# Kernel tuning notes

Measured on AMD Instinct MI355X. Metric: run time of the kernel, lower is better.

The kernel has to match this reference:

```python
import jax, jax.numpy as jnp
import numpy as np

T, H, W, N = 16, 1280, 1280, 64

def setup_inputs() -> dict:
    key = jax.random.key(0)
    k1, k2, k3 = jax.random.split(key, 3)
    result_data = jax.random.normal(k1, (T, H, W), dtype=jnp.float32)
    # boxes: (x1, y1, x2, y2) with x1 <= x2, y1 <= y2 (well-formed, as the torch code assumes)
    xs = jnp.sort(jax.random.randint(k2, (N, 2), 0, W, dtype=jnp.int32), axis=1)
    ys = jnp.sort(jax.random.randint(k3, (N, 2), 0, H, dtype=jnp.int32), axis=1)
    boxes_data = jnp.stack([xs[:, 0], ys[:, 0], xs[:, 1], ys[:, 1]], axis=1)  # [N,4]
    return {"result_data": result_data, "boxes_data": boxes_data}

def reference(result_data, boxes_data):
    # result_data: [T,H,W] float; boxes_data: [N,4] int (x1,y1,x2,y2), exclusive upper bounds.
    # Fuse all per-box region sums via a 2D integral image (summed-area table):
    # S[t, y, x] = sum(result_data[t, :y, :x]); box sum = S[y2,x2]-S[y1,x2]-S[y2,x1]+S[y1,x1].
    cs = jnp.cumsum(jnp.cumsum(result_data, axis=1), axis=2)          # [T,H,W]
    S = jnp.pad(cs, ((0, 0), (1, 0), (1, 0)))                          # [T,H+1,W+1]
    x1, y1, x2, y2 = boxes_data[:, 0], boxes_data[:, 1], boxes_data[:, 2], boxes_data[:, 3]
    box_sums = S[:, y2, x2] - S[:, y1, x2] - S[:, y2, x1] + S[:, y1, x1]  # [T,N]
    return box_sums.sum()
```

## Files before the change

### kernel.cpp

```cpp
#include <hip/hip_runtime.h>

#define TT 16
#define HH 1280
#define WW 1280
#define NBOX 64
#define W4 (WW / 4)
#define SLICE4 (HH * W4)

typedef float f32x4 __attribute__((ext_vector_type(4)));

__global__ void build_masks_kernel(const int* __restrict__ boxes,
                                   unsigned long long* __restrict__ rowmask,
                                   unsigned long long* __restrict__ colmask,
                                   float* __restrict__ out) {
    __shared__ int bx1[NBOX], by1[NBOX], bx2[NBOX], by2[NBOX];
    int tid = threadIdx.x;
    if (tid < NBOX) {
        int4 b = ((const int4*)boxes)[tid];
        bx1[tid] = b.x; by1[tid] = b.y; bx2[tid] = b.z; by2[tid] = b.w;
    }
    if (blockIdx.x == 0 && tid == 0) *out = 0.f;
    __syncthreads();
    int g = blockIdx.x * 256 + tid;
    if (g < HH) {
        int y = g;
        unsigned long long m = 0ull;
#pragma unroll
        for (int b = 0; b < NBOX; ++b)
            if (by1[b] <= y && y < by2[b]) m |= (1ull << b);
        rowmask[y] = m;
    } else if (g < HH + WW) {
        int x = g - HH;
        unsigned long long m = 0ull;
#pragma unroll
        for (int b = 0; b < NBOX; ++b)
            if (bx1[b] <= x && x < bx2[b]) m |= (1ull << b);
        colmask[x] = m;
    }
}

__global__ void __launch_bounds__(256, 6)
weighted_sum_kernel(const f32x4* __restrict__ data,
                    const unsigned long long* __restrict__ rowmask,
                    const longlong2* __restrict__ colmask2,
                    float* __restrict__ out) {
    int idx = blockIdx.x * 256 + threadIdx.x;
    int y  = idx / W4;
    int x4 = idx - y * W4;

    unsigned long long rm = rowmask[y];
    longlong2 c01 = colmask2[x4 * 2 + 0];
    longlong2 c23 = colmask2[x4 * 2 + 1];

    const f32x4* p = data + idx;
    f32x4 v[TT];
#pragma unroll
    for (int t = 0; t < TT; ++t)
        v[t] = __builtin_nontemporal_load(p + t * SLICE4);

    __builtin_amdgcn_sched_barrier(0);

    float w0 = (float)__popcll(rm & (unsigned long long)c01.x);
    float w1 = (float)__popcll(rm & (unsigned long long)c01.y);
    float w2 = (float)__popcll(rm & (unsigned long long)c23.x);
    float w3 = (float)__popcll(rm & (unsigned long long)c23.y);

    float a0 = 0.f, a1 = 0.f, a2 = 0.f, a3 = 0.f;
#pragma unroll
    for (int t = 0; t < TT; t += 4) {
        a0 += v[t + 0].x * w0 + v[t + 0].y * w1 + v[t + 0].z * w2 + v[t + 0].w * w3;
        a1 += v[t + 1].x * w0 + v[t + 1].y * w1 + v[t + 1].z * w2 + v[t + 1].w * w3;
        a2 += v[t + 2].x * w0 + v[t + 2].y * w1 + v[t + 2].z * w2 + v[t + 2].w * w3;
        a3 += v[t + 3].x * w0 + v[t + 3].y * w1 + v[t + 3].z * w2 + v[t + 3].w * w3;
    }
    float acc = (a0 + a1) + (a2 + a3);

#pragma unroll
    for (int off = 32; off > 0; off >>= 1)
        acc += __shfl_down(acc, off, 64);

    __shared__ float wsum[4];
    int lane = threadIdx.x & 63;
    int wid  = threadIdx.x >> 6;
    if (lane == 0) wsum[wid] = acc;
    __syncthreads();
    if (threadIdx.x == 0) {
        float s = (wsum[0] + wsum[1]) + (wsum[2] + wsum[3]);
        atomicAdd(out, s);
    }
}

extern "C" void kernel_launch(void* const* d_in, const int* in_sizes, int n_in,
                              void* d_out, int out_size, void* d_ws, size_t ws_size,
                              hipStream_t stream) {
    const float* data = (const float*)d_in[0];
    const int* boxes  = (const int*)d_in[1];
    float* out = (float*)d_out;

    unsigned long long* rowmask = (unsigned long long*)d_ws;
    unsigned long long* colmask = rowmask + HH;

    build_masks_kernel<<<10, 256, 0, stream>>>(boxes, rowmask, colmask, out);
    weighted_sum_kernel<<<SLICE4 / 256, 256, 0, stream>>>(
        (const f32x4*)data, rowmask, (const longlong2*)colmask, out);
}
```

Measured before the change: 157.9 us.

## Fuse mask build into box-sum kernel, computing per-pixel box counts inline

Drops the separate mask-building kernel and the row/column bitmask workspace. Each thread now loads the 64 boxes into shared memory and counts box coverage for its four pixels in a loop, with the output zeroed by a memset. The data loads switch from nontemporal to plain loads. This saves one launch and the mask reads, but adds about 64 iterations of compare work per thread and an extra memset launch.

```diff
diff --git a/kernel.cpp b/kernel.cpp
--- a/kernel.cpp
+++ b/kernel.cpp
@@ -9,61 +9,39 @@
 
 typedef float f32x4 __attribute__((ext_vector_type(4)));
 
-__global__ void build_masks_kernel(const int* __restrict__ boxes,
-                                   unsigned long long* __restrict__ rowmask,
-                                   unsigned long long* __restrict__ colmask,
-                                   float* __restrict__ out) {
-    __shared__ int bx1[NBOX], by1[NBOX], bx2[NBOX], by2[NBOX];
+__global__ void __launch_bounds__(256, 6)
+fused_boxsum_kernel(const f32x4* __restrict__ data,
+                    const int4* __restrict__ boxes,
+                    float* __restrict__ out) {
+    __shared__ int4 sbox[NBOX];
     int tid = threadIdx.x;
-    if (tid < NBOX) {
-        int4 b = ((const int4*)boxes)[tid];
-        bx1[tid] = b.x; by1[tid] = b.y; bx2[tid] = b.z; by2[tid] = b.w;
-    }
-    if (blockIdx.x == 0 && tid == 0) *out = 0.f;
+    if (tid < NBOX) sbox[tid] = boxes[tid];
     __syncthreads();
-    int g = blockIdx.x * 256 + tid;
-    if (g < HH) {
-        int y = g;
-        unsigned long long m = 0ull;
-#pragma unroll
-        for (int b = 0; b < NBOX; ++b)
-            if (by1[b] <= y && y < by2[b]) m |= (1ull << b);
-        rowmask[y] = m;
-    } else if (g < HH + WW) {
-        int x = g - HH;
-        unsigned long long m = 0ull;
-#pragma unroll
-        for (int b = 0; b < NBOX; ++b)
-            if (bx1[b] <= x && x < bx2[b]) m |= (1ull << b);
-        colmask[x] = m;
-    }
-}
 
-__global__ void __launch_bounds__(256, 6)
-weighted_sum_kernel(const f32x4* __restrict__ data,
-                    const unsigned long long* __restrict__ rowmask,
-                    const longlong2* __restrict__ colmask2,
-                    float* __restrict__ out) {
-    int idx = blockIdx.x * 256 + threadIdx.x;
+    int idx = blockIdx.x * 256 + tid;
     int y  = idx / W4;
     int x4 = idx - y * W4;
-
-    unsigned long long rm = rowmask[y];
-    longlong2 c01 = colmask2[x4 * 2 + 0];
-    longlong2 c23 = colmask2[x4 * 2 + 1];
+    int x0 = x4 * 4;
 
     const f32x4* p = data + idx;
     f32x4 v[TT];
 #pragma unroll
     for (int t = 0; t < TT; ++t)
-        v[t] = __builtin_nontemporal_load(p + t * SLICE4);
+        v[t] = p[t * SLICE4];
 
     __builtin_amdgcn_sched_barrier(0);
 
-    float w0 = (float)__popcll(rm & (unsigned long long)c01.x);
-    float w1 = (float)__popcll(rm & (unsigned long long)c01.y);
-    float w2 = (float)__popcll(rm & (unsigned long long)c23.x);
-    float w3 = (float)__popcll(rm & (unsigned long long)c23.y);
+    int c0 = 0, c1 = 0, c2 = 0, c3 = 0;
+#pragma unroll 2
+    for (int b = 0; b < NBOX; ++b) {
+        int4 bb = sbox[b];
+        int inrow = (bb.y <= y) & (y < bb.w);
+        c0 += inrow & (bb.x <= x0 + 0) & (x0 + 0 < bb.z);
+        c1 += inrow & (bb.x <= x0 + 1) & (x0 + 1 < bb.z);
+        c2 += inrow & (bb.x <= x0 + 2) & (x0 + 2 < bb.z);
+        c3 += inrow & (bb.x <= x0 + 3) & (x0 + 3 < bb.z);
+    }
+    float w0 = (float)c0, w1 = (float)c1, w2 = (float)c2, w3 = (float)c3;
 
     float a0 = 0.f, a1 = 0.f, a2 = 0.f, a3 = 0.f;
 #pragma unroll
@@ -97,10 +75,7 @@
     const int* boxes  = (const int*)d_in[1];
     float* out = (float*)d_out;
 
-    unsigned long long* rowmask = (unsigned long long*)d_ws;
-    unsigned long long* colmask = rowmask + HH;
-
-    build_masks_kernel<<<10, 256, 0, stream>>>(boxes, rowmask, colmask, out);
-    weighted_sum_kernel<<<SLICE4 / 256, 256, 0, stream>>>(
-        (const f32x4*)data, rowmask, (const longlong2*)colmask, out);
+    hipMemsetAsync(out, 0, sizeof(float), stream);
+    fused_boxsum_kernel<<<SLICE4 / 256, 256, 0, stream>>>(
+        (const f32x4*)data, (const int4*)boxes, out);
 }
```

New measurement: 175.8 us. 1.11x slower.
